# Performance work log

Hardware: AMD Instinct MI355X
Metric: run time of the kernel (lower is better)

Reference implementation:

```python
import jax, jax.numpy as jnp
import numpy as np
import math

HIDDEN = 1024
NUM_HEADS = 16
HEAD_DIM = HIDDEN // NUM_HEADS
B, S = 4, 1024


def setup_inputs() -> dict:
    key = jax.random.key(0)
    ks = jax.random.split(key, 16)
    sd = 1.0 / math.sqrt(HIDDEN)
    inp = {
        "x": jax.random.normal(ks[0], (B, S, HIDDEN), jnp.float32),
        "spikes": jax.random.uniform(ks[1], (B, S, HIDDEN), jnp.float32),
        "membrane_potential": jax.random.normal(ks[2], (B, S, HIDDEN), jnp.float32),
        "Wq": jax.random.normal(ks[3], (HIDDEN, HIDDEN), jnp.float32) * sd,
        "bq": jnp.zeros((HIDDEN,), jnp.float32),
        "Wk": jax.random.normal(ks[4], (HIDDEN, HIDDEN), jnp.float32) * sd,
        "bk": jnp.zeros((HIDDEN,), jnp.float32),
        "Wv": jax.random.normal(ks[5], (HIDDEN, HIDDEN), jnp.float32) * sd,
        "bv": jnp.zeros((HIDDEN,), jnp.float32),
        "Wo": jax.random.normal(ks[6], (HIDDEN, HIDDEN), jnp.float32) * sd,
        "bo": jnp.zeros((HIDDEN,), jnp.float32),
        "tau_decay": jnp.ones((NUM_HEADS,), jnp.float32) * 10.0,
        "Wg": jax.random.normal(ks[7], (HIDDEN, 2 * HIDDEN), jnp.float32) * sd,
        "bg": jnp.zeros((HIDDEN,), jnp.float32),
    }
    return inp


def _heads(t):  # [B,S,H] -> [B,nH,S,hd]
    Bv, Sv, _ = t.shape
    return t.reshape(Bv, Sv, NUM_HEADS, HEAD_DIM).transpose(0, 2, 1, 3)


def reference(x, spikes, membrane_potential, Wq, bq, Wk, bk, Wv, bv, Wo, bo, tau_decay, Wg, bg):
    scale = 1.0 / math.sqrt(HEAD_DIM)
    q = _heads(x @ Wq.T + bq)
    k = _heads(x @ Wk.T + bk)
    v = _heads(x @ Wv.T + bv)

    # raw scores [B,nH,S,S]
    scores = jnp.einsum('bhqd,bhkd->bhqk', q, k) * scale

    # per-head exponential temporal decay mask [nH,S,S]
    times = jnp.arange(S, dtype=jnp.float32)
    tdiff = jnp.abs(times[:, None] - times[None, :])  # [S,S]
    tmask = jnp.exp(-tdiff[None] / tau_decay[:, None, None])
    scores = scores * tmask[None]

    # spike correlation term
    sm = _heads(spikes)
    spike_attn = jnp.einsum('bhqd,bhkd->bhqk', sm, sm) * scale
    scores = scores * (1.0 + spike_attn)

    # membrane gating of V
    v = v * jax.nn.sigmoid(_heads(membrane_potential))

    probs = jax.nn.softmax(scores, axis=-1)
    context = jnp.einsum('bhqk,bhkd->bhqd', probs, v)
    context = context.transpose(0, 2, 1, 3).reshape(B, S, HIDDEN)

    # dendritic gate
    gate_in = jnp.concatenate([context, membrane_potential], axis=-1)
    gate = jax.nn.sigmoid(gate_in @ Wg.T + bg)
    context = context * gate

    return context @ Wo.T + bo
```

## Files before the change

### kernel.cpp

```cpp
#include <hip/hip_runtime.h>
#include <math.h>
#include <stdint.h>

namespace {

typedef __attribute__((ext_vector_type(8))) short s8v;
typedef __attribute__((ext_vector_type(4))) float f4v;
typedef unsigned short u16;

__device__ __forceinline__ float fexp2(float x) {
  return __builtin_amdgcn_exp2f(x);
}

__device__ __forceinline__ u16 f2bf(float f) {
  union { float f; uint32_t u; } v; v.f = f;
  uint32_t r = v.u + 0x7fffu + ((v.u >> 16) & 1u);
  return (u16)(r >> 16);
}
__device__ __forceinline__ float bf2f(u16 h) {
  union { uint32_t u; float f; } v; v.u = ((uint32_t)h) << 16;
  return v.f;
}
__device__ __forceinline__ uint32_t pk2r(float a, float b) {
  return (uint32_t)f2bf(a) | ((uint32_t)f2bf(b) << 16);
}
__device__ __forceinline__ uint32_t pk2(float a, float b) {
  union { float f; uint32_t u; } x, y; x.f = a; y.f = b;
  return ((x.u + 0x8000u) >> 16) | ((y.u + 0x8000u) & 0xffff0000u);
}
__device__ __forceinline__ float sigmoidf_(float x) { return 1.0f / (1.0f + __expf(-x)); }

__device__ __forceinline__ void gload16(const u16* g, u16* l) {
  __builtin_amdgcn_global_load_lds(
      (const __attribute__((address_space(1))) void*)g,
      (__attribute__((address_space(3))) void*)l, 16, 0, 0);
}

struct CvtJob { const float* src; u16* dst; };
struct CvtArgs { CvtJob j[18]; float* vz; };

__global__ __launch_bounds__(256) void cvt_kernel(CvtArgs a) {
  if (blockIdx.y == 0 && blockIdx.x < 4) {
    float4 z; z.x = 0.f; z.y = 0.f; z.z = 0.f; z.w = 0.f;
    ((float4*)a.vz)[blockIdx.x * 256 + threadIdx.x] = z;
  }
  const CvtJob jb = a.j[blockIdx.y];
  const int i = blockIdx.x * 256 + threadIdx.x;
  const float4 v = ((const float4*)jb.src)[i];
  uint2 pk;
  pk.x = pk2r(v.x, v.y);
  pk.y = pk2r(v.z, v.w);
  ((uint2*)jb.dst)[i] = pk;
}

__global__ __launch_bounds__(512, 2) void qkv_gemm(
    const u16* __restrict__ xb,
    const u16* __restrict__ Wqb, const u16* __restrict__ Wkb, const u16* __restrict__ Wvb,
    const float* __restrict__ bq, const float* __restrict__ bk, const float* __restrict__ bv,
    const float* __restrict__ mem,
    u16* __restrict__ Qb, u16* __restrict__ Kb, u16* __restrict__ Vt,
    float* __restrict__ Vtot) {
  __shared__ __align__(16) u16 as_[4][4096];
  __shared__ __align__(16) u16 bs_[4][12288];
  const int t = threadIdx.x;
  const int nb = blockIdx.x, mb = blockIdx.y;
  const int m0 = mb * 128, n0 = nb * 128;
  const int l = t & 63, w = t >> 6;
  const int wm = w >> 2, wn = w & 3;
  const int lr = l & 15, lq = l >> 4;
  const int rh = lr >> 1;
  const int rb4 = (lr & 1) << 2;

  const f4v fz = {0.f, 0.f, 0.f, 0.f};
  f4v aq[4][2], ak[4][2], av[4][2];
#pragma unroll
  for (int i = 0; i < 4; ++i)
#pragma unroll
    for (int j = 0; j < 2; ++j) { aq[i][j] = fz; ak[i][j] = fz; av[i][j] = fz; }

  const int tt = t & 255, uu = t >> 8;
  const int sc0 = (tt & 7) ^ ((tt >> 3) & 7);
  const int sgrow = ((tt >> 3) << 1) + (sc0 >> 2);
  const int sgk = (sc0 & 3) << 3;

  const u16* ga = xb + (size_t)(m0 + uu * 64 + sgrow) * 1024 + sgk;
  const u16* gq = Wqb + (size_t)(n0 + uu * 64 + sgrow) * 1024 + sgk;
  const u16* gk = Wkb + (size_t)(n0 + uu * 64 + sgrow) * 1024 + sgk;
  const u16* gv = Wvb + (size_t)(n0 + uu * 64 + sgrow) * 1024 + sgk;
  const int lofs = uu * 2048 + tt * 8;

#define QKV_STAGE(c)                                                           \
  {                                                                            \
    const int ko_ = (c) * 32;                                                  \
    const int bb_ = (c) & 3;                                                   \
    gload16(ga + ko_, &as_[bb_][lofs]);                                        \
    gload16(gq + ko_, &bs_[bb_][lofs]);                                        \
    gload16(gk + ko_, &bs_[bb_][4096 + lofs]);                                 \
    gload16(gv + ko_, &bs_[bb_][8192 + lofs]);                                 \
  }

  QKV_STAGE(0); QKV_STAGE(1); QKV_STAGE(2); QKV_STAGE(3);
  asm volatile("s_waitcnt vmcnt(12)" ::: "memory");
  __builtin_amdgcn_s_barrier();

  const int co = ((rb4 + lq) ^ rh) * 8;
  for (int c = 0; c < 32; ++c) {
    const int cb = c & 3;
    s8v af[4], bfq[2], bfk[2], bfv[2];
#pragma unroll
    for (int mi = 0; mi < 4; ++mi)
      af[mi] = *(const s8v*)(&as_[cb][(wm * 32 + mi * 8 + rh) * 64 + co]);
#pragma unroll
    for (int ni = 0; ni < 2; ++ni) {
      const int ro = (wn * 16 + ni * 8 + rh) * 64 + co;
      bfq[ni] = *(const s8v*)(&bs_[cb][ro]);
      bfk[ni] = *(const s8v*)(&bs_[cb][4096 + ro]);
      bfv[ni] = *(const s8v*)(&bs_[cb][8192 + ro]);
    }
    asm volatile("s_waitcnt lgkmcnt(0)" ::: "memory");
    __builtin_amdgcn_sched_barrier(0);
    __builtin_amdgcn_s_barrier();
    if (c + 4 < 32) QKV_STAGE(c + 4);
    __builtin_amdgcn_s_setprio(1);
#pragma unroll
    for (int mi = 0; mi < 4; ++mi)
#pragma unroll
      for (int ni = 0; ni < 2; ++ni) {
        aq[mi][ni] = __builtin_amdgcn_mfma_f32_16x16x32_bf16(
            bfq[ni], af[mi], aq[mi][ni], 0, 0, 0);
        ak[mi][ni] = __builtin_amdgcn_mfma_f32_16x16x32_bf16(
            bfk[ni], af[mi], ak[mi][ni], 0, 0, 0);
        av[mi][ni] = __builtin_amdgcn_mfma_f32_16x16x32_bf16(
            af[mi], bfv[ni], av[mi][ni], 0, 0, 0);
      }
    __builtin_amdgcn_s_setprio(0);
    if (c < 28) {
      asm volatile("s_waitcnt vmcnt(12)" ::: "memory");
    } else if (c == 28) {
      asm volatile("s_waitcnt vmcnt(8)" ::: "memory");
    } else if (c == 29) {
      asm volatile("s_waitcnt vmcnt(4)" ::: "memory");
    } else if (c == 30) {
      asm volatile("s_waitcnt vmcnt(0)" ::: "memory");
    }
    if (c < 31) __builtin_amdgcn_s_barrier();
  }
#undef QKV_STAGE
  __builtin_amdgcn_sched_barrier(0);

#pragma unroll
  for (int mi = 0; mi < 4; ++mi)
#pragma unroll
    for (int ni = 0; ni < 2; ++ni) {
      const int m = m0 + wm * 64 + mi * 16 + lr;
      const int nb4 = n0 + wn * 32 + ni * 16 + lq * 4;
      const float4 b4 = *(const float4*)&bq[nb4];
      uint2 pk;
      pk.x = pk2r(aq[mi][ni][0] + b4.x, aq[mi][ni][1] + b4.y);
      pk.y = pk2r(aq[mi][ni][2] + b4.z, aq[mi][ni][3] + b4.w);
      *(uint2*)(Qb + (size_t)m * 1024 + nb4) = pk;
    }
#pragma unroll
  for (int mi = 0; mi < 4; ++mi)
#pragma unroll
    for (int ni = 0; ni < 2; ++ni) {
      const int m = m0 + wm * 64 + mi * 16 + lr;
      const int nb4 = n0 + wn * 32 + ni * 16 + lq * 4;
      const float4 b4 = *(const float4*)&bk[nb4];
      uint2 pk;
      pk.x = pk2r(ak[mi][ni][0] + b4.x, ak[mi][ni][1] + b4.y);
      pk.y = pk2r(ak[mi][ni][2] + b4.z, ak[mi][ni][3] + b4.w);
      *(uint2*)(Kb + (size_t)m * 1024 + nb4) = pk;
    }
  {
    const int b = m0 >> 10;
    float vpart[2] = {0.f, 0.f};
#pragma unroll
    for (int mi = 0; mi < 4; ++mi)
#pragma unroll
      for (int ni = 0; ni < 2; ++ni) {
        const int mrow = m0 + wm * 64 + mi * 16 + lq * 4;
        const int ncol = n0 + wn * 32 + ni * 16 + lr;
        const int h = ncol >> 6, d = ncol & 63;
        const float bi = bv[ncol];
        float tv[4];
#pragma unroll
        for (int r = 0; r < 4; ++r)
          tv[r] = (av[mi][ni][r] + bi) * sigmoidf_(mem[(size_t)(mrow + r) * 1024 + ncol]);
        vpart[ni] += (tv[0] + tv[1]) + (tv[2] + tv[3]);
        const int s = mrow & 1023;
        uint2 pk;
        pk.x = pk2r(tv[0], tv[1]);
        pk.y = pk2r(tv[2], tv[3]);
        *(uint2*)(Vt + ((size_t)((b * 16 + h) * 64 + d)) * 1024 + s) = pk;
      }
#pragma unroll
    for (int ni = 0; ni < 2; ++ni) {
      const int ncol = n0 + wn * 32 + ni * 16 + lr;
      atomicAdd(&Vtot[(size_t)(b * 16 + (ncol >> 6)) * 64 + (ncol & 63)], vpart[ni]);
    }
  }
}

template <int MODE>
__global__ __launch_bounds__(256) void gemm64(
    const u16* __restrict__ Ab, const u16* __restrict__ A2b,
    const u16* __restrict__ W, const float* __restrict__ bias,
    u16* __restrict__ outb, float* __restrict__ outf, int K) {
  __shared__ __align__(16) u16 as_[8192], bs_[16384];
  const int t = threadIdx.x, l = t & 63, w = t >> 6;
  const int wm = w >> 1, wn = w & 1, lr = l & 15, lq = l >> 4;
  const int m0 = blockIdx.y * 64, n0 = blockIdx.x * 128;
  const f4v fz = {0.f, 0.f, 0.f, 0.f};
  f4v acc[2][4];
#pragma unroll
  for (int i = 0; i < 2; ++i)
#pragma unroll
    for (int j = 0; j < 4; ++j) acc[i][j] = fz;
  const int rx = lr & 7;
  const int srow = t >> 3;
  const int scol = ((t & 7) ^ (srow & 7)) * 8;
  const int nc = K >> 6;

#define G64_STAGE(k0, bsel)                                                    \
  {                                                                            \
    const int kk_ = (k0);                                                      \
    const u16* Ae_ = Ab;                                                       \
    int ka_ = kk_;                                                             \
    if (MODE == 1 && kk_ >= 1024) { Ae_ = A2b; ka_ = kk_ - 1024; }             \
    _Pragma("unroll") for (int u = 0; u < 2; ++u)                              \
        gload16(Ae_ + (size_t)(m0 + u * 32 + srow) * 1024 + ka_ + scol,        \
                as_ + (bsel) * 4096 + u * 2048 + t * 8);                       \
    _Pragma("unroll") for (int u = 0; u < 4; ++u)                              \
        gload16(W + (size_t)(n0 + u * 32 + srow) * K + kk_ + scol,             \
                bs_ + (bsel) * 8192 + u * 2048 + t * 8);                       \
  }

  G64_STAGE(0, 0);
  G64_STAGE(64, 1);
  asm volatile("s_waitcnt vmcnt(6)" ::: "memory");
  __builtin_amdgcn_s_barrier();

  for (int c = 0; c < nc; ++c) {
    const int pp = c & 1;
    const int loA = pp * 4096, loB = pp * 8192;
    s8v af[2][2], bf[2][4];
#pragma unroll
    for (int ks = 0; ks < 2; ++ks) {
      const int co = ((ks * 4 + lq) ^ rx) * 8;
#pragma unroll
      for (int mi = 0; mi < 2; ++mi)
        af[ks][mi] = *(const s8v*)(as_ + loA + (wm * 32 + mi * 16 + lr) * 64 + co);
#pragma unroll
      for (int ni = 0; ni < 4; ++ni)
        bf[ks][ni] = *(const s8v*)(bs_ + loB + (wn * 64 + ni * 16 + lr) * 64 + co);
    }
    asm volatile("s_waitcnt lgkmcnt(0)" ::: "memory");
    __builtin_amdgcn_sched_barrier(0);
    __builtin_amdgcn_s_barrier();
    if (c + 2 < nc) G64_STAGE((c + 2) << 6, pp);
    __builtin_amdgcn_s_setprio(1);
#pragma unroll
    for (int ks = 0; ks < 2; ++ks)
#pragma unroll
      for (int mi = 0; mi < 2; ++mi)
#pragma unroll
        for (int ni = 0; ni < 4; ++ni)
          acc[mi][ni] = __builtin_amdgcn_mfma_f32_16x16x32_bf16(
              bf[ks][ni], af[ks][mi], acc[mi][ni], 0, 0, 0);
    __builtin_amdgcn_s_setprio(0);
    if (c + 2 < nc) {
      asm volatile("s_waitcnt vmcnt(6)" ::: "memory");
    } else if (c + 1 < nc) {
      asm volatile("s_waitcnt vmcnt(0)" ::: "memory");
    }
    if (c + 1 < nc) __builtin_amdgcn_s_barrier();
  }
  __builtin_amdgcn_sched_barrier(0);
#undef G64_STAGE

#pragma unroll
  for (int mi = 0; mi < 2; ++mi)
#pragma unroll
    for (int ni = 0; ni < 4; ++ni) {
      const int m = m0 + wm * 32 + mi * 16 + lr;
      const int nb4 = n0 + wn * 64 + ni * 16 + lq * 4;
      const float4 b4 = *(const float4*)&bias[nb4];
      if (MODE == 0) {
        float4 o;
        o.x = acc[mi][ni][0] + b4.x; o.y = acc[mi][ni][1] + b4.y;
        o.z = acc[mi][ni][2] + b4.z; o.w = acc[mi][ni][3] + b4.w;
        *(float4*)(outf + (size_t)m * 1024 + nb4) = o;
      } else {
        const uint2 a2 = *(const uint2*)(Ab + (size_t)m * 1024 + nb4);
        float cx[4] = {bf2f((u16)(a2.x & 0xffff)), bf2f((u16)(a2.x >> 16)),
                       bf2f((u16)(a2.y & 0xffff)), bf2f((u16)(a2.y >> 16))};
        float g[4];
        g[0] = cx[0] * sigmoidf_(acc[mi][ni][0] + b4.x);
        g[1] = cx[1] * sigmoidf_(acc[mi][ni][1] + b4.y);
        g[2] = cx[2] * sigmoidf_(acc[mi][ni][2] + b4.z);
        g[3] = cx[3] * sigmoidf_(acc[mi][ni][3] + b4.w);
        uint2 pk;
        pk.x = pk2r(g[0], g[1]);
        pk.y = pk2r(g[2], g[3]);
        *(uint2*)(outb + (size_t)m * 1024 + nb4) = pk;
      }
    }
}

__global__ __launch_bounds__(256) void attn_mfma(
    const u16* __restrict__ Qb, const u16* __restrict__ Kb,
    const u16* __restrict__ SPb, const u16* __restrict__ Vt,
    const float* __restrict__ tau, const float* __restrict__ Vtot,
    u16* __restrict__ CTXb) {
  __shared__ u16 kbuf[4096], skbuf[4096], vbuf[4096];
  __shared__ u16 pbuf[4][16 * 64];
  const int t = threadIdx.x, l = t & 63, w = t >> 6;
  const int lr = l & 15, lq = l >> 4;
  const int p = blockIdx.x;
  const int g = (p & 7) + 8 * (p >> 7);
  const int qt = (p >> 3) & 15;
  const int h = g & 15, b = g >> 4;

  const float tv_ = tau[h];
  const float c2 = 1.44269504088896f / tv_;
  const float K0 = 0.125f * 1.44269504088896f;
  int rad = (int)ceilf(tv_ * 0.171875f);
  if (rad > 15) rad = 15;
  const int jlo = (qt - rad < 0) ? 0 : qt - rad;
  const int jhi = (qt + rad > 15) ? 15 : qt + rad;
  const int farCnt = 16 - (jhi - jlo + 1);

  float cN[4], cNi[4], cR[4], cRi[4];
#pragma unroll
  for (int i = 0; i < 4; ++i) {
    cN[i]  = fexp2(c2 * (float)(i * 16));
    cNi[i] = fexp2(-c2 * (float)(i * 16));
    cR[i]  = fexp2(c2 * (float)(lq * 4 + i));
    cRi[i] = fexp2(-c2 * (float)(lq * 4 + i));
  }

  s8v qf[2], sf[2];
  {
    const size_t base = ((size_t)(b * 1024 + qt * 64 + w * 16 + lr)) * 1024 + h * 64 + lq * 8;
    qf[0] = *(const s8v*)(Qb + base);
    qf[1] = *(const s8v*)(Qb + base + 32);
    sf[0] = *(const s8v*)(SPb + base);
    sf[1] = *(const s8v*)(SPb + base + 32);
  }
  const s8v ones = {0x3F80, 0x3F80, 0x3F80, 0x3F80, 0x3F80, 0x3F80, 0x3F80, 0x3F80};

  const f4v fz = {0.f, 0.f, 0.f, 0.f};
  f4v oacc[4], vs[4];
  float lacc[4];
#pragma unroll
  for (int i = 0; i < 4; ++i) { oacc[i] = fz; vs[i] = fz; lacc[i] = 0.f; }

  const int iqw = qt * 64 + w * 16;
  const int srow = t >> 3;
  const int csw = ((t & 7) ^ (srow & 7)) * 8;
  const int rx = lr & 7;
  u16* pw = pbuf[w];

  for (int jc = jlo; jc <= jhi; ++jc) {
    const int j0 = jc * 64;
    __syncthreads();
    {
      const size_t kg = ((size_t)(b * 1024 + j0 + srow)) * 1024 + h * 64 + csw;
      gload16(Kb + kg, kbuf + t * 8);
      gload16(Kb + kg + 32 * 1024, kbuf + 2048 + t * 8);
      gload16(SPb + kg, skbuf + t * 8);
      gload16(SPb + kg + 32 * 1024, skbuf + 2048 + t * 8);
      const size_t vg = ((size_t)((b * 16 + h) * 64 + srow)) * 1024 + j0 + csw;
      gload16(Vt + vg, vbuf + t * 8);
      gload16(Vt + vg + 32 * 1024, vbuf + 2048 + t * 8);
    }
    __syncthreads();

    f4v sa[4], ssa[4];
#pragma unroll
    for (int ni = 0; ni < 4; ++ni) { sa[ni] = fz; ssa[ni] = fz; }
#pragma unroll
    for (int ks = 0; ks < 2; ++ks) {
#pragma unroll
      for (int ni = 0; ni < 4; ++ni) {
        const int off = (ni * 16 + lr) * 64 + (((ks * 4 + lq) ^ rx) * 8);
        const s8v kf = *(const s8v*)(kbuf + off);
        sa[ni] = __builtin_amdgcn_mfma_f32_16x16x32_bf16(kf, qf[ks], sa[ni], 0, 0, 0);
        const s8v skf = *(const s8v*)(skbuf + off);
        ssa[ni] = __builtin_amdgcn_mfma_f32_16x16x32_bf16(skf, sf[ks], ssa[ni], 0, 0, 0);
      }
    }

    const int D0 = iqw - j0;
    float pv[4][4];
    if (jc < qt) {
      const float EA = K0 * fexp2(-c2 * (float)(D0 + lr));
#pragma unroll
      for (int ni = 0; ni < 4; ++ni)
#pragma unroll
        for (int r = 0; r < 4; ++r) {
          const float t1 = fmaf(ssa[ni][r], 0.125f, 1.0f);
          const float e = fexp2(sa[ni][r] * cN[ni] * cR[r] * EA * t1);
          pv[ni][r] = e;
          lacc[ni] += e;
        }
    } else if (jc > qt) {
      const float EAi = K0 * fexp2(c2 * (float)(D0 + lr));
#pragma unroll
      for (int ni = 0; ni < 4; ++ni)
#pragma unroll
        for (int r = 0; r < 4; ++r) {
          const float t1 = fmaf(ssa[ni][r], 0.125f, 1.0f);
          const float e = fexp2(sa[ni][r] * cNi[ni] * cRi[r] * EAi * t1);
          pv[ni][r] = e;
          lacc[ni] += e;
        }
    } else {
      const float EA  = K0 * fexp2(-c2 * (float)(D0 + lr));
      const float EAi = K0 * fexp2(c2 * (float)(D0 + lr));
#pragma unroll
      for (int ni = 0; ni < 4; ++ni)
#pragma unroll
        for (int r = 0; r < 4; ++r) {
          const int jloc = ni * 16 + lq * 4 + r;
          const float fb = cN[ni] * cR[r] * EA;
          const float fa = cNi[ni] * cRi[r] * EAi;
          const float f = (D0 + lr >= jloc) ? fb : fa;
          const float t1 = fmaf(ssa[ni][r], 0.125f, 1.0f);
          const float e = fexp2(sa[ni][r] * f * t1);
          pv[ni][r] = e;
          lacc[ni] += e;
        }
    }

#pragma unroll
    for (int ni = 0; ni < 4; ++ni) {
      const int phys = (ni * 2 + (lq >> 1)) ^ rx;
      uint2 p2;
      p2.x = pk2(pv[ni][0], pv[ni][1]);
      p2.y = pk2(pv[ni][2], pv[ni][3]);
      *(uint2*)(pw + lr * 64 + phys * 8 + (lq & 1) * 4) = p2;
    }

#pragma unroll
    for (int ks = 0; ks < 2; ++ks) {
      const s8v pf = *(const s8v*)(pw + lr * 64 + (((ks * 4 + lq) ^ rx) * 8));
#pragma unroll
      for (int nd = 0; nd < 4; ++nd) {
        const int off = (nd * 16 + lr) * 64 + (((ks * 4 + lq) ^ rx) * 8);
        const s8v vf = *(const s8v*)(vbuf + off);
        oacc[nd] = __builtin_amdgcn_mfma_f32_16x16x32_bf16(vf, pf, oacc[nd], 0, 0, 0);
        vs[nd] = __builtin_amdgcn_mfma_f32_16x16x32_bf16(vf, ones, vs[nd], 0, 0, 0);
      }
    }
  }

  float ls = (lacc[0] + lacc[1]) + (lacc[2] + lacc[3]);
  ls += __shfl_xor(ls, 16);
  ls += __shfl_xor(ls, 32);
  ls += 64.0f * (float)farCnt;
  const float inv = 1.0f / ls;
  const float* vt0 = Vtot + (size_t)(b * 16 + h) * 64;
  const size_t orow = ((size_t)(b * 1024 + qt * 64 + w * 16 + lr)) * 1024 + h * 64;
#pragma unroll
  for (int nd = 0; nd < 4; ++nd) {
    const float4 vt4 = *(const float4*)(vt0 + nd * 16 + lq * 4);
    float o0 = (oacc[nd][0] + vt4.x - vs[nd][0]) * inv;
    float o1 = (oacc[nd][1] + vt4.y - vs[nd][1]) * inv;
    float o2 = (oacc[nd][2] + vt4.z - vs[nd][2]) * inv;
    float o3 = (oacc[nd][3] + vt4.w - vs[nd][3]) * inv;
    uint2 o;
    o.x = pk2r(o0, o1);
    o.y = pk2r(o2, o3);
    *(uint2*)(CTXb + orow + nd * 16 + lq * 4) = o;
  }
}

}

extern "C" void kernel_launch(void* const* d_in, const int* in_sizes, int n_in,
                              void* d_out, int out_size, void* d_ws, size_t ws_size,
                              hipStream_t stream) {
  const float* x      = (const float*)d_in[0];
  const float* spikes = (const float*)d_in[1];
  const float* mem    = (const float*)d_in[2];
  const float* Wq     = (const float*)d_in[3];
  const float* bq     = (const float*)d_in[4];
  const float* Wk     = (const float*)d_in[5];
  const float* bk     = (const float*)d_in[6];
  const float* Wv     = (const float*)d_in[7];
  const float* bv     = (const float*)d_in[8];
  const float* Wo     = (const float*)d_in[9];
  const float* bo     = (const float*)d_in[10];
  const float* tau    = (const float*)d_in[11];
  const float* Wg     = (const float*)d_in[12];
  const float* bg     = (const float*)d_in[13];
  float* out = (float*)d_out;

  uint8_t* w8 = (uint8_t*)d_ws;
  u16* spb  = (u16*)(w8);
  u16* xb   = (u16*)(w8 + (8u << 20));
  u16* Wqb  = (u16*)(w8 + (16u << 20));
  u16* Wkb  = (u16*)(w8 + (18u << 20));
  u16* Wvb  = (u16*)(w8 + (20u << 20));
  u16* Wob  = (u16*)(w8 + (22u << 20));
  u16* Wgb  = (u16*)(w8 + (24u << 20));
  u16* Qb   = (u16*)(w8 + (28u << 20));
  u16* Kb   = (u16*)(w8 + (36u << 20));
  u16* Vt   = (u16*)(w8 + (44u << 20));
  u16* CTXb = (u16*)(w8 + (52u << 20));
  float* Vtot = (float*)(w8 + (60u << 20));
  u16* memb = (u16*)d_out;
  u16* gctx = xb;

  constexpr size_t QE = 262144 * 4;
  CvtArgs ca;
  for (int q = 0; q < 4; ++q) ca.j[q]     = {x + q * QE,      xb + q * QE};
  for (int q = 0; q < 4; ++q) ca.j[4 + q] = {spikes + q * QE, spb + q * QE};
  for (int q = 0; q < 4; ++q) ca.j[8 + q] = {mem + q * QE,    memb + q * QE};
  ca.j[12] = {Wq, Wqb};
  ca.j[13] = {Wk, Wkb};
  ca.j[14] = {Wv, Wvb};
  ca.j[15] = {Wo, Wob};
  ca.j[16] = {Wg, Wgb};
  ca.j[17] = {Wg + QE, Wgb + QE};
  ca.vz = Vtot;
  cvt_kernel<<<dim3(1024, 18), 256, 0, stream>>>(ca);

  qkv_gemm<<<dim3(8, 32), 512, 0, stream>>>(xb, Wqb, Wkb, Wvb, bq, bk, bv, mem,
                                            Qb, Kb, Vt, Vtot);
  attn_mfma<<<dim3(1024), 256, 0, stream>>>(Qb, Kb, spb, Vt, tau, Vtot, CTXb);
  gemm64<1><<<dim3(8, 64), 256, 0, stream>>>(CTXb, memb, Wgb, bg, gctx, nullptr, 2048);
  gemm64<0><<<dim3(8, 64), 256, 0, stream>>>(gctx, nullptr, Wob, bo, nullptr, out, 1024);
}
```

Baseline: 248.3 us.

## Split QKV pipeline into per-operand phases and retile output GEMMs to 128x128

The QKV GEMM main loop now runs Q, K and V as three phases, each with its own LDS read, barrier and MFMA block. Global prefetch is interleaved per operand at depth 3 instead of one 4-deep stage. The gate and output GEMMs move from 64x128 tiles with 256 threads and 2 K-buffers to 128x128 tiles with 512 threads, a 4-buffer K=32 pipeline and the QKV-style swizzle. This is meant to spread memory traffic across compute and improve reuse per block, at the cost of more barriers and half as many blocks for the output GEMMs.

```diff
diff --git a/kernel.cpp b/kernel.cpp
--- a/kernel.cpp
+++ b/kernel.cpp
@@ -89,54 +89,73 @@
   const u16* gv = Wvb + (size_t)(n0 + uu * 64 + sgrow) * 1024 + sgk;
   const int lofs = uu * 2048 + tt * 8;
 
-#define QKV_STAGE(c)                                                           \
-  {                                                                            \
-    const int ko_ = (c) * 32;                                                  \
-    const int bb_ = (c) & 3;                                                   \
-    gload16(ga + ko_, &as_[bb_][lofs]);                                        \
-    gload16(gq + ko_, &bs_[bb_][lofs]);                                        \
-    gload16(gk + ko_, &bs_[bb_][4096 + lofs]);                                 \
-    gload16(gv + ko_, &bs_[bb_][8192 + lofs]);                                 \
-  }
-
-  QKV_STAGE(0); QKV_STAGE(1); QKV_STAGE(2); QKV_STAGE(3);
-  asm volatile("s_waitcnt vmcnt(12)" ::: "memory");
+#define STAGE_A(c) gload16(ga + (c) * 32, &as_[(c) & 3][lofs])
+#define STAGE_Q(c) gload16(gq + (c) * 32, &bs_[(c) & 3][lofs])
+#define STAGE_K(c) gload16(gk + (c) * 32, &bs_[(c) & 3][4096 + lofs])
+#define STAGE_V(c) gload16(gv + (c) * 32, &bs_[(c) & 3][8192 + lofs])
+
+  STAGE_A(0); STAGE_Q(0); STAGE_K(0); STAGE_V(0);
+  STAGE_A(1); STAGE_Q(1); STAGE_K(1); STAGE_V(1);
+  STAGE_A(2); STAGE_Q(2); STAGE_K(2); STAGE_V(2);
+  asm volatile("s_waitcnt vmcnt(8)" ::: "memory");
   __builtin_amdgcn_s_barrier();
 
   const int co = ((rb4 + lq) ^ rh) * 8;
   for (int c = 0; c < 32; ++c) {
     const int cb = c & 3;
-    s8v af[4], bfq[2], bfk[2], bfv[2];
+    const bool st = (c + 3 < 32);
+    s8v af[4], bq2[2];
 #pragma unroll
     for (int mi = 0; mi < 4; ++mi)
       af[mi] = *(const s8v*)(&as_[cb][(wm * 32 + mi * 8 + rh) * 64 + co]);
 #pragma unroll
-    for (int ni = 0; ni < 2; ++ni) {
-      const int ro = (wn * 16 + ni * 8 + rh) * 64 + co;
-      bfq[ni] = *(const s8v*)(&bs_[cb][ro]);
-      bfk[ni] = *(const s8v*)(&bs_[cb][4096 + ro]);
-      bfv[ni] = *(const s8v*)(&bs_[cb][8192 + ro]);
-    }
+    for (int ni = 0; ni < 2; ++ni)
+      bq2[ni] = *(const s8v*)(&bs_[cb][(wn * 16 + ni * 8 + rh) * 64 + co]);
+    if (st) { STAGE_A(c + 3); STAGE_Q(c + 3); }
+    __builtin_amdgcn_s_barrier();
     asm volatile("s_waitcnt lgkmcnt(0)" ::: "memory");
     __builtin_amdgcn_sched_barrier(0);
+    __builtin_amdgcn_s_setprio(1);
+#pragma unroll
+    for (int mi = 0; mi < 4; ++mi)
+#pragma unroll
+      for (int ni = 0; ni < 2; ++ni)
+        aq[mi][ni] = __builtin_amdgcn_mfma_f32_16x16x32_bf16(
+            bq2[ni], af[mi], aq[mi][ni], 0, 0, 0);
+    __builtin_amdgcn_s_setprio(0);
+    s8v bk2[2];
+#pragma unroll
+    for (int ni = 0; ni < 2; ++ni)
+      bk2[ni] = *(const s8v*)(&bs_[cb][4096 + (wn * 16 + ni * 8 + rh) * 64 + co]);
+    if (st) STAGE_K(c + 3);
     __builtin_amdgcn_s_barrier();
-    if (c + 4 < 32) QKV_STAGE(c + 4);
+    asm volatile("s_waitcnt lgkmcnt(0)" ::: "memory");
+    __builtin_amdgcn_sched_barrier(0);
     __builtin_amdgcn_s_setprio(1);
 #pragma unroll
     for (int mi = 0; mi < 4; ++mi)
 #pragma unroll
-      for (int ni = 0; ni < 2; ++ni) {
-        aq[mi][ni] = __builtin_amdgcn_mfma_f32_16x16x32_bf16(
-            bfq[ni], af[mi], aq[mi][ni], 0, 0, 0);
+      for (int ni = 0; ni < 2; ++ni)
         ak[mi][ni] = __builtin_amdgcn_mfma_f32_16x16x32_bf16(
-            bfk[ni], af[mi], ak[mi][ni], 0, 0, 0);
+            bk2[ni], af[mi], ak[mi][ni], 0, 0, 0);
+    __builtin_amdgcn_s_setprio(0);
+    s8v bv2[2];
+#pragma unroll
+    for (int ni = 0; ni < 2; ++ni)
+      bv2[ni] = *(const s8v*)(&bs_[cb][8192 + (wn * 16 + ni * 8 + rh) * 64 + co]);
+    if (st) STAGE_V(c + 3);
+    __builtin_amdgcn_s_barrier();
+    asm volatile("s_waitcnt lgkmcnt(0)" ::: "memory");
+    __builtin_amdgcn_sched_barrier(0);
+    __builtin_amdgcn_s_setprio(1);
+#pragma unroll
+    for (int mi = 0; mi < 4; ++mi)
+#pragma unroll
+      for (int ni = 0; ni < 2; ++ni)
         av[mi][ni] = __builtin_amdgcn_mfma_f32_16x16x32_bf16(
-            af[mi], bfv[ni], av[mi][ni], 0, 0, 0);
-      }
+            af[mi], bv2[ni], av[mi][ni], 0, 0, 0);
     __builtin_amdgcn_s_setprio(0);
-    if (c < 28) {
-      asm volatile("s_waitcnt vmcnt(12)" ::: "memory");
-    } else if (c == 28) {
+    if (st) {
       asm volatile("s_waitcnt vmcnt(8)" ::: "memory");
     } else if (c == 29) {
       asm volatile("s_waitcnt vmcnt(4)" ::: "memory");
@@ -145,7 +164,10 @@
     }
     if (c < 31) __builtin_amdgcn_s_barrier();
   }
-#undef QKV_STAGE
+#undef STAGE_A
+#undef STAGE_Q
+#undef STAGE_K
+#undef STAGE_V
   __builtin_amdgcn_sched_barrier(0);
 
 #pragma unroll
@@ -203,88 +225,90 @@
 }
 
 template <int MODE>
-__global__ __launch_bounds__(256) void gemm64(
+__global__ __launch_bounds__(512, 2) void gemm64(
     const u16* __restrict__ Ab, const u16* __restrict__ A2b,
     const u16* __restrict__ W, const float* __restrict__ bias,
     u16* __restrict__ outb, float* __restrict__ outf, int K) {
-  __shared__ __align__(16) u16 as_[8192], bs_[16384];
-  const int t = threadIdx.x, l = t & 63, w = t >> 6;
-  const int wm = w >> 1, wn = w & 1, lr = l & 15, lq = l >> 4;
-  const int m0 = blockIdx.y * 64, n0 = blockIdx.x * 128;
+  __shared__ __align__(16) u16 as_[4][4096], bs_[4][4096];
+  const int t = threadIdx.x;
+  const int m0 = blockIdx.y * 128, n0 = blockIdx.x * 128;
+  const int l = t & 63, w = t >> 6;
+  const int wm = w >> 2, wn = w & 3;
+  const int lr = l & 15, lq = l >> 4;
+  const int rh = lr >> 1, rb4 = (lr & 1) << 2;
   const f4v fz = {0.f, 0.f, 0.f, 0.f};
-  f4v acc[2][4];
-#pragma unroll
-  for (int i = 0; i < 2; ++i)
-#pragma unroll
-    for (int j = 0; j < 4; ++j) acc[i][j] = fz;
-  const int rx = lr & 7;
-  const int srow = t >> 3;
-  const int scol = ((t & 7) ^ (srow & 7)) * 8;
-  const int nc = K >> 6;
-
-#define G64_STAGE(k0, bsel)                                                    \
+  f4v acc[4][2];
+#pragma unroll
+  for (int i = 0; i < 4; ++i)
+#pragma unroll
+    for (int j = 0; j < 2; ++j) acc[i][j] = fz;
+
+  const int tt = t & 255, uu = t >> 8;
+  const int sc0 = (tt & 7) ^ ((tt >> 3) & 7);
+  const int sgrow = ((tt >> 3) << 1) + (sc0 >> 2);
+  const int sgk = (sc0 & 3) << 3;
+  const u16* ga1 = Ab + (size_t)(m0 + uu * 64 + sgrow) * 1024 + sgk;
+  const u16* ga2 = (MODE == 1)
+      ? (A2b + (size_t)(m0 + uu * 64 + sgrow) * 1024 + sgk) : ga1;
+  const u16* gw = W + (size_t)(n0 + uu * 64 + sgrow) * K + sgk;
+  const int lofs = uu * 2048 + tt * 8;
+  const int nc = K >> 5;
+
+#define G_STAGE_A(c)                                                           \
   {                                                                            \
-    const int kk_ = (k0);                                                      \
-    const u16* Ae_ = Ab;                                                       \
-    int ka_ = kk_;                                                             \
-    if (MODE == 1 && kk_ >= 1024) { Ae_ = A2b; ka_ = kk_ - 1024; }             \
-    _Pragma("unroll") for (int u = 0; u < 2; ++u)                              \
-        gload16(Ae_ + (size_t)(m0 + u * 32 + srow) * 1024 + ka_ + scol,        \
-                as_ + (bsel) * 4096 + u * 2048 + t * 8);                       \
-    _Pragma("unroll") for (int u = 0; u < 4; ++u)                              \
-        gload16(W + (size_t)(n0 + u * 32 + srow) * K + kk_ + scol,             \
-                bs_ + (bsel) * 8192 + u * 2048 + t * 8);                       \
-  }
-
-  G64_STAGE(0, 0);
-  G64_STAGE(64, 1);
-  asm volatile("s_waitcnt vmcnt(6)" ::: "memory");
+    const int ko_ = (c) * 32;                                                  \
+    if (MODE == 1 && ko_ >= 1024) gload16(ga2 + (ko_ - 1024), &as_[(c) & 3][lofs]); \
+    else gload16(ga1 + ko_, &as_[(c) & 3][lofs]);                              \
+  }
+#define G_STAGE_W(c) gload16(gw + (c) * 32, &bs_[(c) & 3][lofs])
+
+  G_STAGE_A(0); G_STAGE_W(0);
+  G_STAGE_A(1); G_STAGE_W(1);
+  G_STAGE_A(2); G_STAGE_W(2);
+  asm volatile("s_waitcnt vmcnt(4)" ::: "memory");
   __builtin_amdgcn_s_barrier();
 
+  const int co = ((rb4 + lq) ^ rh) * 8;
   for (int c = 0; c < nc; ++c) {
-    const int pp = c & 1;
-    const int loA = pp * 4096, loB = pp * 8192;
-    s8v af[2][2], bf[2][4];
-#pragma unroll
-    for (int ks = 0; ks < 2; ++ks) {
-      const int co = ((ks * 4 + lq) ^ rx) * 8;
-#pragma unroll
-      for (int mi = 0; mi < 2; ++mi)
-        af[ks][mi] = *(const s8v*)(as_ + loA + (wm * 32 + mi * 16 + lr) * 64 + co);
-#pragma unroll
-      for (int ni = 0; ni < 4; ++ni)
-        bf[ks][ni] = *(const s8v*)(bs_ + loB + (wn * 64 + ni * 16 + lr) * 64 + co);
-    }
+    const int cb = c & 3;
+    s8v af[4], bf[2];
+#pragma unroll
+    for (int mi = 0; mi < 4; ++mi)
+      af[mi] = *(const s8v*)(&as_[cb][(wm * 32 + mi * 8 + rh) * 64 + co]);
+#pragma unroll
+    for (int ni = 0; ni < 2; ++ni)
+      bf[ni] = *(const s8v*)(&bs_[cb][(wn * 16 + ni * 8 + rh) * 64 + co]);
+    if (c + 3 < nc) { G_STAGE_A(c + 3); G_STAGE_W(c + 3); }
+    __builtin_amdgcn_s_barrier();
     asm volatile("s_waitcnt lgkmcnt(0)" ::: "memory");
     __builtin_amdgcn_sched_barrier(0);
-    __builtin_amdgcn_s_barrier();
-    if (c + 2 < nc) G64_STAGE((c + 2) << 6, pp);
     __builtin_amdgcn_s_setprio(1);
 #pragma unroll
-    for (int ks = 0; ks < 2; ++ks)
-#pragma unroll
-      for (int mi = 0; mi < 2; ++mi)
-#pragma unroll
-        for (int ni = 0; ni < 4; ++ni)
-          acc[mi][ni] = __builtin_amdgcn_mfma_f32_16x16x32_bf16(
-              bf[ks][ni], af[ks][mi], acc[mi][ni], 0, 0, 0);
+    for (int mi = 0; mi < 4; ++mi)
+#pragma unroll
+      for (int ni = 0; ni < 2; ++ni)
+        acc[mi][ni] = __builtin_amdgcn_mfma_f32_16x16x32_bf16(
+            bf[ni], af[mi], acc[mi][ni], 0, 0, 0);
     __builtin_amdgcn_s_setprio(0);
-    if (c + 2 < nc) {
-      asm volatile("s_waitcnt vmcnt(6)" ::: "memory");
-    } else if (c + 1 < nc) {
+    if (c + 3 < nc) {
+      asm volatile("s_waitcnt vmcnt(4)" ::: "memory");
+    } else if (c + 3 == nc) {
+      asm volatile("s_waitcnt vmcnt(2)" ::: "memory");
+    } else if (c + 2 == nc) {
       asm volatile("s_waitcnt vmcnt(0)" ::: "memory");
     }
     if (c + 1 < nc) __builtin_amdgcn_s_barrier();
   }
+#undef G_STAGE_A
+#undef G_STAGE_W
   __builtin_amdgcn_sched_barrier(0);
-#undef G64_STAGE
-
-#pragma unroll
-  for (int mi = 0; mi < 2; ++mi)
-#pragma unroll
-    for (int ni = 0; ni < 4; ++ni) {
-      const int m = m0 + wm * 32 + mi * 16 + lr;
-      const int nb4 = n0 + wn * 64 + ni * 16 + lq * 4;
+
+#pragma unroll
+  for (int mi = 0; mi < 4; ++mi)
+#pragma unroll
+    for (int ni = 0; ni < 2; ++ni) {
+      const int m = m0 + wm * 64 + mi * 16 + lr;
+      const int nb4 = n0 + wn * 32 + ni * 16 + lq * 4;
       const float4 b4 = *(const float4*)&bias[nb4];
       if (MODE == 0) {
         float4 o;
@@ -531,6 +555,6 @@
   qkv_gemm<<<dim3(8, 32), 512, 0, stream>>>(xb, Wqb, Wkb, Wvb, bq, bk, bv, mem,
                                             Qb, Kb, Vt, Vtot);
   attn_mfma<<<dim3(1024), 256, 0, stream>>>(Qb, Kb, spb, Vt, tau, Vtot, CTXb);
-  gemm64<1><<<dim3(8, 64), 256, 0, stream>>>(CTXb, memb, Wgb, bg, gctx, nullptr, 2048);
-  gemm64<0><<<dim3(8, 64), 256, 0, stream>>>(gctx, nullptr, Wob, bo, nullptr, out, 1024);
-}
+  gemm64<1><<<dim3(8, 32), 512, 0, stream>>>(CTXb, memb, Wgb, bg, gctx, nullptr, 2048);
+  gemm64<0><<<dim3(8, 32), 512, 0, stream>>>(gctx, nullptr, Wob, bo, nullptr, out, 1024);
+}
```

New measurement: 253.9 us. 1.02x slower.
